# Kernel tuning notes

Hardware: AMD Instinct MI355X
Metric: run time of the kernel (lower is better)

The kernel has to match this reference:

```python
import jax, jax.numpy as jnp
import numpy as np

H = 1024      # hidden_size
I = 4096      # intermediate_size (4*H SwiGLU)
E = 8         # num_experts
TOPK = 2      # num_experts_per_tok


def setup_inputs() -> dict:
    key = jax.random.key(0)
    ks = jax.random.split(key, 6)
    B, S = 4, 2048
    hidden_states = jax.random.normal(ks[0], (B, S, H), dtype=jnp.float32)
    # router gate (no bias)
    gate_w = jax.random.normal(ks[1], (H, E), dtype=jnp.float32) * (1.0 / np.sqrt(H))
    # per-expert SwiGLU weights (xavier-ish scale)
    W1 = jax.random.normal(ks[2], (E, H, I), dtype=jnp.float32) * np.sqrt(2.0 / (H + I))
    W3 = jax.random.normal(ks[3], (E, H, I), dtype=jnp.float32) * np.sqrt(2.0 / (H + I))
    W2 = jax.random.normal(ks[4], (E, I, H), dtype=jnp.float32) * np.sqrt(2.0 / (H + I))
    # per-expert domain embedding (added to expert input), init std 0.02
    dom = jax.random.normal(ks[5], (E, H), dtype=jnp.float32) * 0.02
    return {"hidden_states": hidden_states, "gate_w": gate_w,
            "W1": W1, "W2": W2, "W3": W3, "dom": dom}


def reference(hidden_states, gate_w, W1, W2, W3, dom):
    B, S, Hd = hidden_states.shape
    x = hidden_states.reshape(-1, Hd)                      # [T, H]
    router_logits = x @ gate_w                             # [T, E]
    top_logits, top_idx = jax.lax.top_k(router_logits, TOPK)
    weights = jax.nn.softmax(top_logits, axis=-1)          # [T, K]
    # dense per-(token, expert) combine weight; 0 for unselected experts
    w_dense = jnp.einsum('tk,tke->te', weights,
                         jax.nn.one_hot(top_idx, E, dtype=weights.dtype))  # [T, E]
    out = jnp.zeros_like(x)
    for e in range(E):  # small fixed expert loop (structurally distinct weights)
        xe = x + dom[e]                                    # domain embedding add
        h = jax.nn.silu(xe @ W1[e]) * (xe @ W3[e])         # SwiGLU [T, I]
        out = out + w_dense[:, e:e + 1] * (h @ W2[e])      # weighted combine
    return out.reshape(B, S, Hd)
```

## Files before the change

kernel.cpp:

```cpp
#include <hip/hip_runtime.h>
#include <hip/hip_bf16.h>
#include <stdint.h>

#define T_TOK 8192
#define H_DIM 1024
#define I_DIM 4096
#define NEXP  8
#define BM    128
#define FBK   64
#define RT_TILES 136
#define RMAX (RT_TILES * BM)

typedef __attribute__((ext_vector_type(8))) short bf16x8;
typedef __attribute__((ext_vector_type(4))) float f32x4;

__device__ __forceinline__ unsigned short f2bf(float f) {
    unsigned int u = __float_as_uint(f);
    return (unsigned short)((u + 0x7FFFu + ((u >> 16) & 1u)) >> 16);
}
__device__ __forceinline__ unsigned int pk2(float a, float b) {
    return (unsigned int)f2bf(a) | ((unsigned int)f2bf(b) << 16);
}
__device__ __forceinline__ void gl_lds16(const void* g, void* l) {
    __builtin_amdgcn_global_load_lds(
        (const __attribute__((address_space(1))) unsigned int*)g,
        (__attribute__((address_space(3))) unsigned int*)l, 16, 0, 0);
}

__global__ __launch_bounds__(256) void router_k(const float* __restrict__ x,
                                                const float* __restrict__ gw,
                                                int2* __restrict__ ridx,
                                                float2* __restrict__ rw) {
    __shared__ float gwT[NEXP][H_DIM + 8];
    for (int i = threadIdx.x; i < H_DIM * NEXP; i += 256) {
        const int k = i >> 3, e = i & 7;
        gwT[e][k] = gw[i];
    }
    __syncthreads();
    const int wid = threadIdx.x >> 6, lane = threadIdx.x & 63;
    const int t = blockIdx.x * 4 + wid;
    const float4* xr = (const float4*)(x + (size_t)t * H_DIM);
    float acc[NEXP];
#pragma unroll
    for (int e = 0; e < NEXP; ++e) acc[e] = 0.f;
#pragma unroll
    for (int jj = 0; jj < 4; ++jj) {
        const float4 v = xr[jj * 64 + lane];
        const int kb = jj * 256 + lane * 4;
#pragma unroll
        for (int e = 0; e < NEXP; ++e) {
            const float4 g = *(const float4*)&gwT[e][kb];
            acc[e] += v.x * g.x + v.y * g.y + v.z * g.z + v.w * g.w;
        }
    }
#pragma unroll
    for (int e = 0; e < NEXP; ++e) {
#pragma unroll
        for (int off = 32; off > 0; off >>= 1) acc[e] += __shfl_xor(acc[e], off, 64);
    }
    if (lane == 0) {
        int i0 = 0; float l0 = acc[0];
#pragma unroll
        for (int e = 1; e < NEXP; ++e) if (acc[e] > l0) { l0 = acc[e]; i0 = e; }
        int i1 = -1; float l1 = -3.4e38f;
#pragma unroll
        for (int e = 0; e < NEXP; ++e) if (e != i0 && acc[e] > l1) { l1 = acc[e]; i1 = e; }
        float ee = __expf(l1 - l0);
        float w0 = 1.f / (1.f + ee);
        float w1 = 1.f - w0;
        ridx[t] = make_int2(i0, i1);
        rw[t]   = make_float2(w0, w1);
    }
}

__global__ __launch_bounds__(256) void plan_k(const int2* __restrict__ ridx,
                                              int* __restrict__ offs,
                                              int* __restrict__ rpos) {
    __shared__ int cnt[256][NEXP];
    __shared__ int base_sh[256][NEXP];
    __shared__ int tot_sh[NEXP];
    __shared__ int offs_sh[NEXP + 1];
    const int tid = threadIdx.x;
    const int t0 = tid * (T_TOK / 256);
    int c[NEXP];
#pragma unroll
    for (int e = 0; e < NEXP; ++e) c[e] = 0;
    for (int j = 0; j < T_TOK / 256; ++j) {
        const int2 ii = ridx[t0 + j];
#pragma unroll
        for (int e = 0; e < NEXP; ++e)
            c[e] += (ii.x == e ? 1 : 0) + (ii.y == e ? 1 : 0);
    }
#pragma unroll
    for (int e = 0; e < NEXP; ++e) cnt[tid][e] = c[e];
    __syncthreads();
    if (tid < NEXP) {
        int s = 0;
        for (int i = 0; i < 256; ++i) s += cnt[i][tid];
        tot_sh[tid] = s;
    }
    __syncthreads();
    if (tid == 0) {
        int o = 0;
#pragma unroll
        for (int e = 0; e < NEXP; ++e) {
            offs_sh[e] = o; offs[e] = o;
            o += (tot_sh[e] + BM - 1) & ~(BM - 1);
        }
        offs_sh[NEXP] = o; offs[NEXP] = o;
    }
    __syncthreads();
    if (tid < NEXP) {
        int run = offs_sh[tid];
        for (int i = 0; i < 256; ++i) {
            base_sh[i][tid] = run;
            run += cnt[i][tid];
        }
    }
    __syncthreads();
    int b[NEXP];
#pragma unroll
    for (int e = 0; e < NEXP; ++e) b[e] = base_sh[tid][e];
    for (int j = 0; j < T_TOK / 256; ++j) {
        const int2 ii = ridx[t0 + j];
        int r0 = 0, r1 = 0;
#pragma unroll
        for (int e = 0; e < NEXP; ++e) r0 += (ii.x == e ? b[e] : 0);
#pragma unroll
        for (int e = 0; e < NEXP; ++e) b[e] += (ii.x == e ? 1 : 0);
#pragma unroll
        for (int e = 0; e < NEXP; ++e) r1 += (ii.y == e ? b[e] : 0);
#pragma unroll
        for (int e = 0; e < NEXP; ++e) b[e] += (ii.y == e ? 1 : 0);
        rpos[2 * (t0 + j)]     = r0;
        rpos[2 * (t0 + j) + 1] = r1;
    }
}

__global__ __launch_bounds__(256) void scatter_w13t_k(
        const float* __restrict__ x, const float* __restrict__ dom,
        const int2* __restrict__ ridx, const float2* __restrict__ rw,
        const int* __restrict__ rpos, float* __restrict__ rwgt,
        unsigned short* __restrict__ xg,
        const float* __restrict__ W1, const float* __restrict__ W3,
        unsigned short* __restrict__ w13) {
    __shared__ float st[64 * 65];
    if (blockIdx.x < 2048) {
        const int wid = threadIdx.x >> 6, lane = threadIdx.x & 63;
        const int t = blockIdx.x * 4 + wid;
        const int2 ii = ridx[t];
        const float2 ww = rw[t];
        const int r0 = rpos[2 * t], r1 = rpos[2 * t + 1];
        if (lane == 0) {
            rwgt[r0] = ww.x;
            rwgt[r1] = ww.y;
        }
        const float4* xr = (const float4*)(x + (size_t)t * H_DIM);
        float4 xv[4];
#pragma unroll
        for (int jj = 0; jj < 4; ++jj) xv[jj] = xr[jj * 64 + lane];
#pragma unroll
        for (int s = 0; s < 2; ++s) {
            const int e = s ? ii.y : ii.x;
            const int rr = s ? r1 : r0;
            const float4* dr = (const float4*)(dom + (size_t)e * H_DIM);
            unsigned short* op = xg + (size_t)rr * H_DIM;
#pragma unroll
            for (int jj = 0; jj < 4; ++jj) {
                const float4 b = dr[jj * 64 + lane];
                const int kb = jj * 256 + lane * 4;
                *(uint2*)(op + kb) = make_uint2(pk2(xv[jj].x + b.x, xv[jj].y + b.y),
                                                pk2(xv[jj].z + b.z, xv[jj].w + b.w));
            }
        }
    } else {
        const int idx = blockIdx.x - 2048;
        const int nt = idx & 63;
        const int kt = (idx >> 6) & 15;
        const int z  = idx >> 10;
        const int e = z >> 1, sel = z & 1;
        const float* src = (sel ? W3 : W1) + (size_t)e * H_DIM * I_DIM;
        const int t = threadIdx.x;
        const int kr = t >> 2, c0 = (t & 3) << 4;
        const float* sp = src + (size_t)(kt * 64 + kr) * I_DIM + nt * 64 + c0;
#pragma unroll
        for (int j = 0; j < 4; ++j) {
            float4 v = *(const float4*)(sp + j * 4);
            st[kr * 65 + c0 + j*4 + 0] = v.x; st[kr * 65 + c0 + j*4 + 1] = v.y;
            st[kr * 65 + c0 + j*4 + 2] = v.z; st[kr * 65 + c0 + j*4 + 3] = v.w;
        }
        __syncthreads();
        const int nl = t >> 2, k0 = (t & 3) << 4;
        const int n = nt * 64 + nl;
        const size_t drow = (size_t)e * 8192 + (size_t)((n >> 4) << 5) + (sel << 4) + (n & 15);
        unsigned short* dp = w13 + drow * H_DIM + kt * 64 + k0;
        unsigned int pk[8];
#pragma unroll
        for (int j = 0; j < 8; ++j)
            pk[j] = pk2(st[(k0 + 2*j) * 65 + nl], st[(k0 + 2*j + 1) * 65 + nl]);
        *(uint4*)dp = make_uint4(pk[0], pk[1], pk[2], pk[3]);
        *(uint4*)(dp + 8) = make_uint4(pk[4], pk[5], pk[6], pk[7]);
    }
}

__global__ __launch_bounds__(256, 4) void gemm1_w2t_k(
        const unsigned short* __restrict__ xg,
        const unsigned short* __restrict__ w13,
        const int* __restrict__ offs,
        unsigned short* __restrict__ h,
        const float* __restrict__ W2,
        unsigned short* __restrict__ w2t) {
    __shared__ unsigned short smem[2 * BM * FBK];
    if (blockIdx.x < 8704) {
        unsigned short* As = smem;
        unsigned short* Bs = smem + BM * FBK;
        const int wg = blockIdx.x;
        const int bx = wg & 63, by = wg >> 6;
        const int r0 = by * BM;
        if (r0 >= offs[NEXP]) return;
        int e = 0;
#pragma unroll
        for (int i = 1; i < NEXP; ++i) if (offs[i] <= r0) e = i;

        const int t = threadIdx.x, wid = t >> 6, lane = t & 63;
        const int srow = wid * 8 + (lane >> 3);
        const int schunk = (lane & 7) ^ (lane >> 3);
        const unsigned short* Agp = xg + (size_t)(r0 + srow) * H_DIM + (schunk << 3);
        const unsigned short* Bgp = w13 + ((size_t)e * 8192 + bx * 128 + srow) * H_DIM + (schunk << 3);
        unsigned short* Al = As + wid * 512;
        unsigned short* Bl = Bs + wid * 512;

        const int fr = lane & 15, g = lane >> 4, h3 = lane & 7;
        const int wr = (wid >> 1) * 64, wc = (wid & 1) * 64;

        f32x4 acc[4][4];
#pragma unroll
        for (int m = 0; m < 4; ++m)
#pragma unroll
            for (int n = 0; n < 4; ++n) acc[m][n] = (f32x4){0.f, 0.f, 0.f, 0.f};

#pragma unroll 1
        for (int kt = 0; kt < H_DIM / FBK; ++kt) {
            __syncthreads();
#pragma unroll
            for (int i = 0; i < 4; ++i) {
                gl_lds16(Agp + kt * FBK + i * 32 * H_DIM, Al + i * 2048);
                gl_lds16(Bgp + kt * FBK + i * 32 * H_DIM, Bl + i * 2048);
            }
            __syncthreads();
#pragma unroll
            for (int s = 0; s < 2; ++s) {
                const int pc = (((s << 2) + g) ^ h3) << 3;
                bf16x8 a[4], b[4];
#pragma unroll
                for (int m = 0; m < 4; ++m)
                    a[m] = *(const bf16x8*)&As[(wr + m * 16 + fr) * FBK + pc];
#pragma unroll
                for (int n = 0; n < 4; ++n)
                    b[n] = *(const bf16x8*)&Bs[(wc + n * 16 + fr) * FBK + pc];
#pragma unroll
                for (int m = 0; m < 4; ++m)
#pragma unroll
                    for (int n = 0; n < 4; ++n)
                        acc[m][n] = __builtin_amdgcn_mfma_f32_16x16x32_bf16(a[m], b[n], acc[m][n], 0, 0, 0);
            }
        }
        const int colbase = bx * 64 + ((wc >> 5) << 4) + fr;
#pragma unroll
        for (int m = 0; m < 4; ++m) {
            const int rbase = r0 + wr + m * 16 + (g << 2);
#pragma unroll
            for (int q = 0; q < 4; ++q) {
                unsigned short* hp = h + (size_t)(rbase + q) * I_DIM;
#pragma unroll
                for (int p = 0; p < 2; ++p) {
                    float p1 = acc[m][2 * p][q], p3 = acc[m][2 * p + 1][q];
                    float sv = p1 / (1.f + __expf(-p1));
                    hp[colbase + p * 16] = f2bf(sv * p3);
                }
            }
        }
    } else {
        float* st = (float*)smem;
        const int idx = blockIdx.x - 8704;
        const int nt = idx & 15;
        const int kt = (idx >> 4) & 63;
        const int e  = idx >> 10;
        const float* src = W2 + (size_t)e * I_DIM * H_DIM;
        const int t = threadIdx.x;
        const int kr = t >> 2, c0 = (t & 3) << 4;
        const float* sp = src + (size_t)(kt * 64 + kr) * H_DIM + nt * 64 + c0;
#pragma unroll
        for (int j = 0; j < 4; ++j) {
            float4 v = *(const float4*)(sp + j * 4);
            st[kr * 65 + c0 + j*4 + 0] = v.x; st[kr * 65 + c0 + j*4 + 1] = v.y;
            st[kr * 65 + c0 + j*4 + 2] = v.z; st[kr * 65 + c0 + j*4 + 3] = v.w;
        }
        __syncthreads();
        const int nl = t >> 2, k0 = (t & 3) << 4;
        unsigned short* dp = w2t + ((size_t)e * 1024 + nt * 64 + nl) * I_DIM + kt * 64 + k0;
        unsigned int pk[8];
#pragma unroll
        for (int j = 0; j < 8; ++j)
            pk[j] = pk2(st[(k0 + 2*j) * 65 + nl], st[(k0 + 2*j + 1) * 65 + nl]);
        *(uint4*)dp = make_uint4(pk[0], pk[1], pk[2], pk[3]);
        *(uint4*)(dp + 8) = make_uint4(pk[4], pk[5], pk[6], pk[7]);
    }
}

__global__ __launch_bounds__(256, 4) void gemm2_ksplit_k(
        const unsigned short* __restrict__ hbuf,
        const unsigned short* __restrict__ w2t,
        const int* __restrict__ offs,
        float* __restrict__ y) {
    __shared__ unsigned short As[BM * FBK];
    __shared__ unsigned short Bs[BM * FBK];
    const int bid = blockIdx.x;
    const int ks = (bid >= 1088) ? 1 : 0;
    const int sb = bid - ks * 1088;
    const int idx = sb >> 3;
    const int by = (sb & 7) * 17 + (idx >> 3);
    const int bx = idx & 7;
    const int r0 = by * BM;
    if (r0 >= offs[NEXP]) return;
    int e = 0;
#pragma unroll
    for (int i = 1; i < NEXP; ++i) if (offs[i] <= r0) e = i;

    const int t = threadIdx.x, wid = t >> 6, lane = t & 63;
    const int srow = wid * 8 + (lane >> 3);
    const int schunk = (lane & 7) ^ (lane >> 3);
    const unsigned short* Agp = hbuf + (size_t)(r0 + srow) * I_DIM + (schunk << 3);
    const unsigned short* Bgp = w2t + ((size_t)e * 1024 + bx * 128 + srow) * I_DIM + (schunk << 3);
    unsigned short* Al = &As[wid * 512];
    unsigned short* Bl = &Bs[wid * 512];

    const int fr = lane & 15, g = lane >> 4, h3 = lane & 7;
    const int wr = (wid >> 1) * 64, wc = (wid & 1) * 64;

    f32x4 acc[4][4];
#pragma unroll
    for (int m = 0; m < 4; ++m)
#pragma unroll
        for (int n = 0; n < 4; ++n) acc[m][n] = (f32x4){0.f, 0.f, 0.f, 0.f};

    const int kt0 = ks * 32;
#pragma unroll 1
    for (int kt = kt0; kt < kt0 + 32; ++kt) {
        __syncthreads();
#pragma unroll
        for (int i = 0; i < 4; ++i) {
            gl_lds16(Agp + kt * FBK + (size_t)i * 32 * I_DIM, Al + i * 2048);
            gl_lds16(Bgp + kt * FBK + (size_t)i * 32 * I_DIM, Bl + i * 2048);
        }
        __syncthreads();
#pragma unroll
        for (int s = 0; s < 2; ++s) {
            const int pcc = (((s << 2) + g) ^ h3) << 3;
            bf16x8 av[4], bv[4];
#pragma unroll
            for (int m = 0; m < 4; ++m)
                av[m] = *(const bf16x8*)&As[(wr + m * 16 + fr) * FBK + pcc];
#pragma unroll
            for (int n = 0; n < 4; ++n)
                bv[n] = *(const bf16x8*)&Bs[(wc + n * 16 + fr) * FBK + pcc];
#pragma unroll
            for (int m = 0; m < 4; ++m)
#pragma unroll
                for (int n = 0; n < 4; ++n)
                    acc[m][n] = __builtin_amdgcn_mfma_f32_16x16x32_bf16(av[m], bv[n], acc[m][n], 0, 0, 0);
        }
    }
    float* yo = y + (size_t)ks * ((size_t)RMAX * H_DIM);
#pragma unroll
    for (int m = 0; m < 4; ++m) {
#pragma unroll
        for (int q = 0; q < 4; ++q) {
            const int rr = r0 + wr + m * 16 + (g << 2) + q;
            float* yp = yo + (size_t)rr * H_DIM + bx * 128 + wc + fr;
#pragma unroll
            for (int n = 0; n < 4; ++n) yp[n * 16] = acc[m][n][q];
        }
    }
}

__global__ __launch_bounds__(256) void combine_k(const float* __restrict__ y,
                                                 const int* __restrict__ rpos,
                                                 const float* __restrict__ rwgt,
                                                 float* __restrict__ out) {
    const float* y1 = y + (size_t)RMAX * H_DIM;
    const int wid = threadIdx.x >> 6, lane = threadIdx.x & 63;
    const int t = blockIdx.x * 4 + wid;
    const int ra = rpos[2 * t], rb = rpos[2 * t + 1];
    const float wa = rwgt[ra], wb = rwgt[rb];
    const f32x4* pa0 = (const f32x4*)(y  + (size_t)ra * H_DIM);
    const f32x4* pa1 = (const f32x4*)(y1 + (size_t)ra * H_DIM);
    const f32x4* pb0 = (const f32x4*)(y  + (size_t)rb * H_DIM);
    const f32x4* pb1 = (const f32x4*)(y1 + (size_t)rb * H_DIM);
    f32x4* po = (f32x4*)(out + (size_t)t * H_DIM);
#pragma unroll
    for (int j = 0; j < 4; ++j) {
        const int i = lane + j * 64;
        const f32x4 a0 = pa0[i], a1 = pa1[i], b0 = pb0[i], b1 = pb1[i];
        const f32x4 r = wa * (a0 + a1) + wb * (b0 + b1);
        __builtin_nontemporal_store(r, po + i);
    }
}

#define WS_OFFS  0
#define WS_RIDX  256
#define WS_RW    (WS_RIDX + T_TOK * 8)
#define WS_RWGT  (WS_RW + T_TOK * 8)
#define WS_RPOS  (WS_RWGT + RMAX * 4)
#define WS_W13   266752
#define WS_XG    (WS_W13 + (size_t)134217728)
#define WS_W2T   (WS_XG + (size_t)RMAX * H_DIM * 2)
#define WS_H     (WS_W2T + (size_t)67108864)
#define WS_Y     WS_W13

extern "C" void kernel_launch(void* const* d_in, const int* in_sizes, int n_in,
                              void* d_out, int out_size, void* d_ws, size_t ws_size,
                              hipStream_t stream) {
    (void)in_sizes; (void)n_in; (void)ws_size; (void)out_size;
    const float* x   = (const float*)d_in[0];
    const float* gw  = (const float*)d_in[1];
    const float* W1  = (const float*)d_in[2];
    const float* W2  = (const float*)d_in[3];
    const float* W3  = (const float*)d_in[4];
    const float* dom = (const float*)d_in[5];
    float* out = (float*)d_out;

    char* ws = (char*)d_ws;
    int*    offs   = (int*)(ws + WS_OFFS);
    int2*   ridx   = (int2*)(ws + WS_RIDX);
    float2* rw     = (float2*)(ws + WS_RW);
    float*  rwgt   = (float*)(ws + WS_RWGT);
    int*    rpos   = (int*)(ws + WS_RPOS);
    unsigned short* w13 = (unsigned short*)(ws + WS_W13);
    unsigned short* xg  = (unsigned short*)(ws + WS_XG);
    unsigned short* w2t = (unsigned short*)(ws + WS_W2T);
    unsigned short* hb  = (unsigned short*)(ws + WS_H);
    float*          y   = (float*)(ws + WS_Y);

    router_k<<<T_TOK / 4, 256, 0, stream>>>(x, gw, ridx, rw);
    plan_k<<<1, 256, 0, stream>>>(ridx, offs, rpos);
    scatter_w13t_k<<<2048 + 16384, 256, 0, stream>>>(x, dom, ridx, rw, rpos, rwgt, xg,
                                                     W1, W3, w13);
    gemm1_w2t_k<<<8704 + 8192, 256, 0, stream>>>(xg, w13, offs, hb, W2, w2t);
    gemm2_ksplit_k<<<2176, 256, 0, stream>>>(hb, w2t, offs, y);
    combine_k<<<T_TOK / 4, 256, 0, stream>>>(y, rpos, rwgt, out);
}
```

Measured before the change: 604.9 us.

## Enlarge gemm1 M tile to 256 rows with per-expert tile table

The first grouped GEMM now uses 256-row M tiles (each wave computes 128x64) so every weight tile loaded from w13 is reused across twice as many token rows. plan_k builds a tile table of (row start, expert, row end) per expert segment, since segments are padded only to 128 rows. Partial tiles clamp their loads and mask their stores. This halves weight traffic and block count in gemm1, at the cost of doubled accumulator registers, occupancy lowered to 2 blocks per SIMD group, and some wasted MFMA work on half-empty tiles.

```diff
diff --git a/kernel.cpp b/kernel.cpp
--- a/kernel.cpp
+++ b/kernel.cpp
@@ -10,6 +10,7 @@
 #define FBK   64
 #define RT_TILES 136
 #define RMAX (RT_TILES * BM)
+#define NTILE_MAX 72
 
 typedef __attribute__((ext_vector_type(8))) short bf16x8;
 typedef __attribute__((ext_vector_type(4))) float f32x4;
@@ -75,7 +76,8 @@
 
 __global__ __launch_bounds__(256) void plan_k(const int2* __restrict__ ridx,
                                               int* __restrict__ offs,
-                                              int* __restrict__ rpos) {
+                                              int* __restrict__ rpos,
+                                              int* __restrict__ tinfo) {
     __shared__ int cnt[256][NEXP];
     __shared__ int base_sh[256][NEXP];
     __shared__ int tot_sh[NEXP];
@@ -108,6 +110,17 @@
             o += (tot_sh[e] + BM - 1) & ~(BM - 1);
         }
         offs_sh[NEXP] = o; offs[NEXP] = o;
+        int ntl = 0;
+        for (int e2 = 0; e2 < NEXP; ++e2) {
+            const int oe = offs_sh[e2], on = offs_sh[e2 + 1];
+            for (int r = oe; r < on; r += 256) {
+                tinfo[1 + ntl] = r;
+                tinfo[1 + NTILE_MAX + ntl] = e2;
+                tinfo[1 + 2 * NTILE_MAX + ntl] = (r + 256 < on) ? r + 256 : on;
+                ++ntl;
+            }
+        }
+        tinfo[0] = ntl;
     }
     __syncthreads();
     if (tid < NEXP) {
@@ -203,39 +216,43 @@
     }
 }
 
-__global__ __launch_bounds__(256, 4) void gemm1_w2t_k(
+__global__ __launch_bounds__(256, 2) void gemm1_w2t_k(
         const unsigned short* __restrict__ xg,
         const unsigned short* __restrict__ w13,
-        const int* __restrict__ offs,
+        const int* __restrict__ tinfo,
         unsigned short* __restrict__ h,
         const float* __restrict__ W2,
         unsigned short* __restrict__ w2t) {
-    __shared__ unsigned short smem[2 * BM * FBK];
-    if (blockIdx.x < 8704) {
+    __shared__ unsigned short smem[3 * BM * FBK];
+    if (blockIdx.x < 4608) {
         unsigned short* As = smem;
-        unsigned short* Bs = smem + BM * FBK;
-        const int wg = blockIdx.x;
-        const int bx = wg & 63, by = wg >> 6;
-        const int r0 = by * BM;
-        if (r0 >= offs[NEXP]) return;
-        int e = 0;
-#pragma unroll
-        for (int i = 1; i < NEXP; ++i) if (offs[i] <= r0) e = i;
+        unsigned short* Bs = smem + 2 * BM * FBK;
+        const int by = blockIdx.x >> 6, bx = blockIdx.x & 63;
+        if (by >= tinfo[0]) return;
+        const int r0   = tinfo[1 + by];
+        const int e    = tinfo[1 + NTILE_MAX + by];
+        const int rend = tinfo[1 + 2 * NTILE_MAX + by];
 
         const int t = threadIdx.x, wid = t >> 6, lane = t & 63;
         const int srow = wid * 8 + (lane >> 3);
         const int schunk = (lane & 7) ^ (lane >> 3);
-        const unsigned short* Agp = xg + (size_t)(r0 + srow) * H_DIM + (schunk << 3);
+        const unsigned short* Agp[8];
+#pragma unroll
+        for (int i = 0; i < 8; ++i) {
+            int rr = r0 + srow + i * 32;
+            if (rr > RMAX - 1) rr = RMAX - 1;
+            Agp[i] = xg + (size_t)rr * H_DIM + (schunk << 3);
+        }
         const unsigned short* Bgp = w13 + ((size_t)e * 8192 + bx * 128 + srow) * H_DIM + (schunk << 3);
         unsigned short* Al = As + wid * 512;
         unsigned short* Bl = Bs + wid * 512;
 
         const int fr = lane & 15, g = lane >> 4, h3 = lane & 7;
-        const int wr = (wid >> 1) * 64, wc = (wid & 1) * 64;
-
-        f32x4 acc[4][4];
-#pragma unroll
-        for (int m = 0; m < 4; ++m)
+        const int wr = (wid >> 1) * 128, wc = (wid & 1) * 64;
+
+        f32x4 acc[8][4];
+#pragma unroll
+        for (int m = 0; m < 8; ++m)
 #pragma unroll
             for (int n = 0; n < 4; ++n) acc[m][n] = (f32x4){0.f, 0.f, 0.f, 0.f};
 
@@ -243,23 +260,24 @@
         for (int kt = 0; kt < H_DIM / FBK; ++kt) {
             __syncthreads();
 #pragma unroll
-            for (int i = 0; i < 4; ++i) {
-                gl_lds16(Agp + kt * FBK + i * 32 * H_DIM, Al + i * 2048);
+            for (int i = 0; i < 8; ++i)
+                gl_lds16(Agp[i] + kt * FBK, Al + i * 2048);
+#pragma unroll
+            for (int i = 0; i < 4; ++i)
                 gl_lds16(Bgp + kt * FBK + i * 32 * H_DIM, Bl + i * 2048);
-            }
             __syncthreads();
 #pragma unroll
             for (int s = 0; s < 2; ++s) {
                 const int pc = (((s << 2) + g) ^ h3) << 3;
-                bf16x8 a[4], b[4];
-#pragma unroll
-                for (int m = 0; m < 4; ++m)
+                bf16x8 a[8], b[4];
+#pragma unroll
+                for (int m = 0; m < 8; ++m)
                     a[m] = *(const bf16x8*)&As[(wr + m * 16 + fr) * FBK + pc];
 #pragma unroll
                 for (int n = 0; n < 4; ++n)
                     b[n] = *(const bf16x8*)&Bs[(wc + n * 16 + fr) * FBK + pc];
 #pragma unroll
-                for (int m = 0; m < 4; ++m)
+                for (int m = 0; m < 8; ++m)
 #pragma unroll
                     for (int n = 0; n < 4; ++n)
                         acc[m][n] = __builtin_amdgcn_mfma_f32_16x16x32_bf16(a[m], b[n], acc[m][n], 0, 0, 0);
@@ -267,22 +285,25 @@
         }
         const int colbase = bx * 64 + ((wc >> 5) << 4) + fr;
 #pragma unroll
-        for (int m = 0; m < 4; ++m) {
+        for (int m = 0; m < 8; ++m) {
             const int rbase = r0 + wr + m * 16 + (g << 2);
 #pragma unroll
             for (int q = 0; q < 4; ++q) {
-                unsigned short* hp = h + (size_t)(rbase + q) * I_DIM;
-#pragma unroll
-                for (int p = 0; p < 2; ++p) {
-                    float p1 = acc[m][2 * p][q], p3 = acc[m][2 * p + 1][q];
-                    float sv = p1 / (1.f + __expf(-p1));
-                    hp[colbase + p * 16] = f2bf(sv * p3);
+                const int rr2 = rbase + q;
+                if (rr2 < rend) {
+                    unsigned short* hp = h + (size_t)rr2 * I_DIM;
+#pragma unroll
+                    for (int p = 0; p < 2; ++p) {
+                        float p1 = acc[m][2 * p][q], p3 = acc[m][2 * p + 1][q];
+                        float sv = p1 / (1.f + __expf(-p1));
+                        hp[colbase + p * 16] = f2bf(sv * p3);
+                    }
                 }
             }
         }
     } else {
         float* st = (float*)smem;
-        const int idx = blockIdx.x - 8704;
+        const int idx = blockIdx.x - 4608;
         const int nt = idx & 15;
         const int kt = (idx >> 4) & 63;
         const int e  = idx >> 10;
@@ -408,11 +429,12 @@
 }
 
 #define WS_OFFS  0
-#define WS_RIDX  256
+#define WS_TILE  256
+#define WS_RIDX  1280
 #define WS_RW    (WS_RIDX + T_TOK * 8)
 #define WS_RWGT  (WS_RW + T_TOK * 8)
 #define WS_RPOS  (WS_RWGT + RMAX * 4)
-#define WS_W13   266752
+#define WS_W13   267520
 #define WS_XG    (WS_W13 + (size_t)134217728)
 #define WS_W2T   (WS_XG + (size_t)RMAX * H_DIM * 2)
 #define WS_H     (WS_W2T + (size_t)67108864)
@@ -432,6 +454,7 @@
 
     char* ws = (char*)d_ws;
     int*    offs   = (int*)(ws + WS_OFFS);
+    int*    tinfo  = (int*)(ws + WS_TILE);
     int2*   ridx   = (int2*)(ws + WS_RIDX);
     float2* rw     = (float2*)(ws + WS_RW);
     float*  rwgt   = (float*)(ws + WS_RWGT);
@@ -443,10 +466,10 @@
     float*          y   = (float*)(ws + WS_Y);
 
     router_k<<<T_TOK / 4, 256, 0, stream>>>(x, gw, ridx, rw);
-    plan_k<<<1, 256, 0, stream>>>(ridx, offs, rpos);
+    plan_k<<<1, 256, 0, stream>>>(ridx, offs, rpos, tinfo);
     scatter_w13t_k<<<2048 + 16384, 256, 0, stream>>>(x, dom, ridx, rw, rpos, rwgt, xg,
                                                      W1, W3, w13);
-    gemm1_w2t_k<<<8704 + 8192, 256, 0, stream>>>(xg, w13, offs, hb, W2, w2t);
+    gemm1_w2t_k<<<4608 + 8192, 256, 0, stream>>>(xg, w13, tinfo, hb, W2, w2t);
     gemm2_ksplit_k<<<2176, 256, 0, stream>>>(hb, w2t, offs, y);
     combine_k<<<T_TOK / 4, 256, 0, stream>>>(y, rpos, rwgt, out);
 }
```

New measurement: 657.8 us. +8.7%, slower.
